# Performance work log

Hardware: AMD Instinct MI355X
Metric: run time of the kernel (lower is better)

## Reference

```python
import jax, jax.numpy as jnp
import numpy as np

BATCH, IN_DIM, HID, OUT_DIM, Z = 8192, 2048, 4096, 2048, 4
CONN_P = 0.5  # Bernoulli keep-probability y


def random_activation(h, ids):
    # ids: [dim] int32 in [0,5); per-channel nonlinearity applied over batch.
    ids = ids[None, :]
    return jnp.select(
        [ids == 0, ids == 1, ids == 2, ids == 3],
        [jax.nn.relu(h), jax.nn.sigmoid(h), jnp.tanh(h), jnp.where(h >= 0, h, 0.1 * h)],
        jax.nn.selu(h),
    )


def _make_linear(key, fan_in, fan_out):
    kw, kb, km = jax.random.split(key, 3)
    w = jax.random.normal(kw, (fan_out, fan_in), dtype=jnp.float32)
    mask = jax.random.bernoulli(km, CONN_P, (fan_out, fan_in)).astype(jnp.float32)
    b = jax.random.normal(kb, (fan_out,), dtype=jnp.float32)
    return w * mask, b


def setup_inputs() -> dict:
    key = jax.random.key(0)
    ks = jax.random.split(key, 16)
    inp = {"input_pattern": jax.random.normal(ks[0], (BATCH, IN_DIM), dtype=jnp.float32)}
    dims = [(IN_DIM, HID)] + [(HID, HID)] * Z + [(HID, OUT_DIM)]  # z+2 Linear layers
    for i, (fi, fo) in enumerate(dims):
        w, b = _make_linear(ks[1 + i], fi, fo)
        inp[f"w{i}"] = w
        inp[f"b{i}"] = b
        inp[f"ids{i}"] = jax.random.randint(ks[8 + i], (fo,), 0, 5, dtype=jnp.int32)
    return inp


def reference(input_pattern, w0, b0, ids0, w1, b1, ids1, w2, b2, ids2,
              w3, b3, ids3, w4, b4, ids4, w5, b5, ids5):
    ws = (w0, w1, w2, w3, w4, w5)
    bs = (b0, b1, b2, b3, b4, b5)
    ids = (ids0, ids1, ids2, ids3, ids4, ids5)
    h = input_pattern
    for w, b, i in zip(ws, bs, ids):
        h = random_activation(h @ w.T + b, i)
    return h
```

## Files before the change

### kernel.cpp

```cpp
#include <hip/hip_runtime.h>

typedef _Float16 f16;
typedef _Float16 f16x8 __attribute__((ext_vector_type(8)));
typedef float f32x4 __attribute__((ext_vector_type(4)));

#define BM 256
#define BN 256
#define BK 32

__device__ __forceinline__ void gload_lds16(const void* g, void* l) {
  __builtin_amdgcn_global_load_lds(
      (const __attribute__((address_space(1))) void*)g,
      (__attribute__((address_space(3))) void*)l, 16, 0, 0);
}

__device__ __forceinline__ float act_apply(float x, int id) {
  switch (id) {
    case 0: return fmaxf(x, 0.0f);
    case 1: return 1.0f / (1.0f + __expf(-x));
    case 2: return tanhf(x);
    case 3: return x >= 0.0f ? x : 0.1f * x;
    default: return 1.0507009873554805f *
                    (x > 0.0f ? x : 1.6732632423543772f * expm1f(x));
  }
}

template <bool FINAL>
__global__ __launch_bounds__(512, 2)
void gemm_bias_act(const f16* __restrict__ A, const f16* __restrict__ W,
                   const float* __restrict__ bias, const int* __restrict__ ids,
                   float Sa, float invSn, void* __restrict__ outv,
                   int M, int N, int K) {
  __shared__ f16 lA[4][BM * BK];
  __shared__ f16 lB[4][BN * BK];

  const int tid  = (int)threadIdx.x;
  const int lane = tid & 63;
  const int wid  = tid >> 6;
  const int wm   = wid >> 2;
  const int wn   = wid & 3;

  const int nbx = N >> 8;
  const int nwg = (M >> 8) * nbx;
  const int b   = (int)blockIdx.x;
  const int swz = (b & 7) * (nwg >> 3) + (b >> 3);
  const int brow = (swz / nbx) << 8;
  const int bcol = (swz % nbx) << 8;

  const int d0 = tid << 4;
  const int d1 = d0 + 8192;
  const int s0 = d0 ^ (((d0 >> 7) & 7) << 4);
  const int s1 = d1 ^ (((d1 >> 7) & 7) << 4);
  const int r0 = s0 >> 6, c0 = (s0 >> 4) & 3;
  const int r1 = s1 >> 6, c1 = (s1 >> 4) & 3;

  const f16* pA0 = A + (long)(brow + r0) * K + c0 * 8;
  const f16* pA1 = A + (long)(brow + r1) * K + c1 * 8;
  const f16* pB0 = W + (long)(bcol + r0) * K + c0 * 8;
  const f16* pB1 = W + (long)(bcol + r1) * K + c1 * 8;
  const int e0 = tid << 3;
  const int e1 = e0 + 4096;

#define STAGE(t)                                    \
  do {                                              \
    const int _s = (t) & 3;                         \
    const long _k = (long)(t) << 5;                 \
    gload_lds16(pA0 + _k, &lA[_s][e0]);             \
    gload_lds16(pA1 + _k, &lA[_s][e1]);             \
    gload_lds16(pB0 + _k, &lB[_s][e0]);             \
    gload_lds16(pB1 + _k, &lB[_s][e1]);             \
  } while (0)

  const int fr = lane & 15;
  const int kb = lane >> 4;
  const int xorv = ((fr >> 1) & 7) << 4;
  const char* baA = (const char*)&lA[0][0];
  const char* baB = (const char*)&lB[0][0];

  int offA[8], offB[4];
#pragma unroll
  for (int m = 0; m < 8; ++m)
    offA[m] = (((wm * 128 + m * 16 + fr) << 6) + (kb << 4)) ^ xorv;
#pragma unroll
  for (int n = 0; n < 4; ++n)
    offB[n] = (((wn * 64 + n * 16 + fr) << 6) + (kb << 4)) ^ xorv;

  f32x4 acc[8][4];
#pragma unroll
  for (int m = 0; m < 8; ++m)
#pragma unroll
    for (int n = 0; n < 4; ++n) acc[m][n] = (f32x4){0.f, 0.f, 0.f, 0.f};

  const int nt = K >> 5;

  STAGE(0);
  STAGE(1);
  STAGE(2);

  for (int i = 0; i < nt; ++i) {
    if (i + 3 < nt) {
      STAGE(i + 3);
      asm volatile("s_waitcnt vmcnt(12)" ::: "memory");
    } else if (nt - 1 - i == 2) {
      asm volatile("s_waitcnt vmcnt(8)" ::: "memory");
    } else if (nt - 1 - i == 1) {
      asm volatile("s_waitcnt vmcnt(4)" ::: "memory");
    } else {
      asm volatile("s_waitcnt vmcnt(0)" ::: "memory");
    }
    __builtin_amdgcn_s_barrier();
    asm volatile("" ::: "memory");

    const int so = (i & 3) << 14;
    f16x8 af[8], bf[4];
#pragma unroll
    for (int m = 0; m < 8; ++m)
      af[m] = *(const f16x8*)(baA + so + offA[m]);
#pragma unroll
    for (int n = 0; n < 4; ++n)
      bf[n] = *(const f16x8*)(baB + so + offB[n]);

    __builtin_amdgcn_s_setprio(1);
#pragma unroll
    for (int m = 0; m < 8; ++m)
#pragma unroll
      for (int n = 0; n < 4; ++n)
        acc[m][n] = __builtin_amdgcn_mfma_f32_16x16x32_f16(af[m], bf[n],
                                                           acc[m][n], 0, 0, 0);
    __builtin_amdgcn_s_setprio(0);

    asm volatile("" ::: "memory");
    __builtin_amdgcn_s_barrier();
  }
#undef STAGE

  const int r4 = (lane >> 4) << 2;
#pragma unroll
  for (int n = 0; n < 4; ++n) {
    const int gcol = bcol + wn * 64 + n * 16 + fr;
    const float bv = bias[gcol];
    const int id   = ids[gcol];
#pragma unroll
    for (int m = 0; m < 8; ++m) {
      const int grow = brow + wm * 128 + m * 16 + r4;
#pragma unroll
      for (int i = 0; i < 4; ++i) {
        const float y = act_apply(acc[m][n][i] * Sa + bv, id);
        if (FINAL) {
          ((float*)outv)[(long)(grow + i) * N + gcol] = y;
        } else {
          ((f16*)outv)[(long)(grow + i) * N + gcol] = (f16)(y * invSn);
        }
      }
    }
  }
}

__global__ void cvt_f32_to_f16(const float* __restrict__ in, f16* __restrict__ out,
                               float scale, int n) {
  int i = ((int)blockIdx.x * 256 + (int)threadIdx.x) * 8;
  const int stride = (int)gridDim.x * 256 * 8;
  for (; i < n; i += stride) {
    const float4 v0 = *(const float4*)(in + i);
    const float4 v1 = *(const float4*)(in + i + 4);
    f16x8 h;
    h[0] = (f16)(v0.x * scale); h[1] = (f16)(v0.y * scale);
    h[2] = (f16)(v0.z * scale); h[3] = (f16)(v0.w * scale);
    h[4] = (f16)(v1.x * scale); h[5] = (f16)(v1.y * scale);
    h[6] = (f16)(v1.z * scale); h[7] = (f16)(v1.w * scale);
    *(f16x8*)(out + i) = h;
  }
}

extern "C" void kernel_launch(void* const* d_in, const int* in_sizes, int n_in,
                              void* d_out, int out_size, void* d_ws, size_t ws_size,
                              hipStream_t stream) {
  (void)in_sizes; (void)n_in; (void)out_size; (void)ws_size;
  const int M = 8192, IND = 2048, HID = 4096, OUTD = 2048;
  const float* x = (const float*)d_in[0];

  f16* actA = (f16*)d_ws;
  f16* actB = actA + (size_t)M * HID;
  f16* wbuf = actB + (size_t)M * HID;

  const float S[6] = {1.f, 16.f, 512.f, 16384.f, 262144.f, 8388608.f};

  const int Ks[6] = {IND, HID, HID, HID, HID, HID};
  const int Ns[6] = {HID, HID, HID, HID, HID, OUTD};

  cvt_f32_to_f16<<<2048, 256, 0, stream>>>(x, actA, 1.0f, M * IND);

  f16* cur = actA;
  f16* nxt = actB;
  for (int i = 0; i < 6; ++i) {
    const int K = Ks[i], N = Ns[i];
    const float* w  = (const float*)d_in[1 + 3 * i];
    const float* bs = (const float*)d_in[2 + 3 * i];
    const int* id   = (const int*)d_in[3 + 3 * i];

    cvt_f32_to_f16<<<2048, 256, 0, stream>>>(w, wbuf, 1.0f, N * K);

    const int nblk = (M >> 8) * (N >> 8);
    if (i < 5) {
      gemm_bias_act<false><<<nblk, 512, 0, stream>>>(
          cur, wbuf, bs, id, S[i], 1.0f / S[i + 1], nxt, M, N, K);
      f16* t = cur; cur = nxt; nxt = t;
    } else {
      gemm_bias_act<true><<<nblk, 512, 0, stream>>>(
          cur, wbuf, bs, id, S[i], 1.0f, d_out, M, N, K);
    }
  }
}
```

Measured before the change: 2.214 ms.

## Split MFMA loop into two half-tiles interleaving LDS reads and global prefetch

Restructures the GEMM main loop so each K-step runs as two halves of MFMAs. The LDS fragment reads for the next half, or the next K-step, and the split global-to-LDS prefetches are issued between them, so LDS and global traffic overlap with matrix-core work instead of sitting before it. This adds extra barriers per iteration and more intricate vmcnt bookkeeping, which risks stalls or ordering mistakes.

```diff
diff --git a/kernel.cpp b/kernel.cpp
--- a/kernel.cpp
+++ b/kernel.cpp
@@ -3,10 +3,6 @@
 typedef _Float16 f16;
 typedef _Float16 f16x8 __attribute__((ext_vector_type(8)));
 typedef float f32x4 __attribute__((ext_vector_type(4)));
-
-#define BM 256
-#define BN 256
-#define BK 32
 
 __device__ __forceinline__ void gload_lds16(const void* g, void* l) {
   __builtin_amdgcn_global_load_lds(
@@ -31,8 +27,8 @@
                    const float* __restrict__ bias, const int* __restrict__ ids,
                    float Sa, float invSn, void* __restrict__ outv,
                    int M, int N, int K) {
-  __shared__ f16 lA[4][BM * BK];
-  __shared__ f16 lB[4][BN * BK];
+  __shared__ f16 lA[4][256 * 32];
+  __shared__ f16 lB[4][256 * 32];
 
   const int tid  = (int)threadIdx.x;
   const int lane = tid & 63;
@@ -61,16 +57,6 @@
   const int e0 = tid << 3;
   const int e1 = e0 + 4096;
 
-#define STAGE(t)                                    \
-  do {                                              \
-    const int _s = (t) & 3;                         \
-    const long _k = (long)(t) << 5;                 \
-    gload_lds16(pA0 + _k, &lA[_s][e0]);             \
-    gload_lds16(pA1 + _k, &lA[_s][e1]);             \
-    gload_lds16(pB0 + _k, &lB[_s][e0]);             \
-    gload_lds16(pB1 + _k, &lB[_s][e1]);             \
-  } while (0)
-
   const int fr = lane & 15;
   const int kb = lane >> 4;
   const int xorv = ((fr >> 1) & 7) << 4;
@@ -93,46 +79,82 @@
 
   const int nt = K >> 5;
 
-  STAGE(0);
-  STAGE(1);
-  STAGE(2);
+#pragma unroll
+  for (int t = 0; t < 3; ++t) {
+    const long kk = (long)t << 5;
+    gload_lds16(pA0 + kk, &lA[t][e0]);
+    gload_lds16(pA1 + kk, &lA[t][e1]);
+    gload_lds16(pB0 + kk, &lB[t][e0]);
+    gload_lds16(pB1 + kk, &lB[t][e1]);
+  }
+  asm volatile("s_waitcnt vmcnt(8)" ::: "memory");
+  __builtin_amdgcn_s_barrier();
+  asm volatile("" ::: "memory");
+
+  f16x8 afA[4], afB[4], bf[4];
+#pragma unroll
+  for (int m = 0; m < 4; ++m) afA[m] = *(const f16x8*)(baA + offA[m]);
+#pragma unroll
+  for (int n = 0; n < 4; ++n) bf[n]  = *(const f16x8*)(baB + offB[n]);
 
   for (int i = 0; i < nt; ++i) {
-    if (i + 3 < nt) {
-      STAGE(i + 3);
-      asm volatile("s_waitcnt vmcnt(12)" ::: "memory");
-    } else if (nt - 1 - i == 2) {
-      asm volatile("s_waitcnt vmcnt(8)" ::: "memory");
-    } else if (nt - 1 - i == 1) {
-      asm volatile("s_waitcnt vmcnt(4)" ::: "memory");
-    } else {
-      asm volatile("s_waitcnt vmcnt(0)" ::: "memory");
-    }
+    const int so  = (i & 3) << 14;
+    const int so2 = ((i + 1) & 3) << 14;
+    const int ps  = (i + 3) & 3;
+    const long kk3 = (long)(i + 3) << 5;
+    const bool pf = (i + 3) < nt;
+
+#pragma unroll
+    for (int m = 0; m < 4; ++m)
+      afB[m] = *(const f16x8*)(baA + so + offA[m + 4]);
+    if (pf) {
+      gload_lds16(pA0 + kk3, &lA[ps][e0]);
+      gload_lds16(pB0 + kk3, &lB[ps][e0]);
+    }
+    __builtin_amdgcn_s_setprio(1);
+#pragma unroll
+    for (int m = 0; m < 4; ++m)
+#pragma unroll
+      for (int n = 0; n < 4; ++n)
+        acc[m][n] = __builtin_amdgcn_mfma_f32_16x16x32_f16(afA[m], bf[n],
+                                                           acc[m][n], 0, 0, 0);
+    __builtin_amdgcn_s_setprio(0);
+    asm volatile("" ::: "memory");
     __builtin_amdgcn_s_barrier();
     asm volatile("" ::: "memory");
 
-    const int so = (i & 3) << 14;
-    f16x8 af[8], bf[4];
-#pragma unroll
-    for (int m = 0; m < 8; ++m)
-      af[m] = *(const f16x8*)(baA + so + offA[m]);
-#pragma unroll
-    for (int n = 0; n < 4; ++n)
-      bf[n] = *(const f16x8*)(baB + so + offB[n]);
-
+    if (i < nt - 1) {
+      if (i < nt - 3)       asm volatile("s_waitcnt vmcnt(6)" ::: "memory");
+      else if (i == nt - 3) asm volatile("s_waitcnt vmcnt(4)" ::: "memory");
+      else                  asm volatile("s_waitcnt vmcnt(0)" ::: "memory");
+      __builtin_amdgcn_s_barrier();
+      asm volatile("" ::: "memory");
+    }
     __builtin_amdgcn_s_setprio(1);
 #pragma unroll
-    for (int m = 0; m < 8; ++m)
+    for (int m = 0; m < 4; ++m)
 #pragma unroll
       for (int n = 0; n < 4; ++n)
-        acc[m][n] = __builtin_amdgcn_mfma_f32_16x16x32_f16(af[m], bf[n],
-                                                           acc[m][n], 0, 0, 0);
+        acc[4 + m][n] = __builtin_amdgcn_mfma_f32_16x16x32_f16(afB[m], bf[n],
+                                                               acc[4 + m][n],
+                                                               0, 0, 0);
     __builtin_amdgcn_s_setprio(0);
-
-    asm volatile("" ::: "memory");
-    __builtin_amdgcn_s_barrier();
-  }
-#undef STAGE
+    if (i < nt - 1) {
+#pragma unroll
+      for (int m = 0; m < 4; ++m)
+        afA[m] = *(const f16x8*)(baA + so2 + offA[m]);
+#pragma unroll
+      for (int n = 0; n < 4; ++n)
+        bf[n] = *(const f16x8*)(baB + so2 + offB[n]);
+      if (pf) {
+        gload_lds16(pA1 + kk3, &lA[ps][e1]);
+        gload_lds16(pB1 + kk3, &lB[ps][e1]);
+      }
+      asm volatile("" ::: "memory");
+      __builtin_amdgcn_s_barrier();
+      asm volatile("" ::: "memory");
+    }
+  }
 
   const int r4 = (lane >> 4) << 2;
 #pragma unroll
```

New measurement: 1.951 ms. -11.9%, faster.
